# Kernel tuning notes

Hardware: AMD Instinct MI355X
Metric: run time of the kernel (lower is better)

The kernel has to match this reference:

```python
import jax, jax.numpy as jnp
import numpy as np

N_ENT, N_REL, H, DEG, TOPK = 150000, 500, 128, 32, 10


def setup_inputs() -> dict:
    key = jax.random.key(0)
    ks = jax.random.split(key, 8)
    return {
        "ent_emb": jax.random.normal(ks[0], (N_ENT, H), jnp.float32),
        "rel_emb": jax.random.normal(ks[1], (N_REL, H), jnp.float32),
        "W": jax.random.normal(ks[2], (H, H), jnp.float32) * 0.1,
        "W_r": jax.random.normal(ks[3], (H, H), jnp.float32) * 0.1,
        "a": jax.random.normal(ks[4], (3 * H, 1), jnp.float32) * 0.1,
        "neigh_w": jax.random.normal(ks[5], (H, H), jnp.float32) * 0.1,
        "src": jax.random.randint(ks[6], (N_ENT, DEG), 0, N_ENT),      # src node of each in-edge per dst
        "rel_id": jax.random.randint(ks[7], (N_ENT, DEG), 0, N_REL),   # relation id per edge
    }


def reference(ent_emb, rel_emb, W, W_r, a, neigh_w, src, rel_id):
    # node / relation projections
    h_node = ent_emb @ W                    # [N_ENT, H]
    h_rel = rel_emb @ W_r                   # [N_REL, H]
    # split attention vector: leaky_relu([h_src|h_dst|r] @ a) == leaky_relu(h_src@a1 + h_dst@a2 + r@a3)
    a1, a2, a3 = a[:H, 0], a[H:2 * H, 0], a[2 * H:, 0]
    s_src = h_node @ a1                     # [N_ENT]
    s_dst = h_node @ a2                     # [N_ENT]
    s_rel = h_rel @ a3                      # [N_REL]

    # edge scores on full graph; dst of row i is node i
    score = jax.nn.leaky_relu(s_src[src] + s_dst[:, None] + s_rel[rel_id], 0.2)  # [N_ENT, DEG]

    # top-k incoming edges per destination (dgl.sampling.select_topk, edge_dir='in')
    _, top_idx = jax.lax.top_k(score, TOPK)                 # [N_ENT, TOPK]
    src_k = jnp.take_along_axis(src, top_idx, axis=1)       # [N_ENT, TOPK]
    rel_k = jnp.take_along_axis(rel_id, top_idx, axis=1)

    # recompute attention on sampled subgraph + edge softmax per destination
    e = jax.nn.leaky_relu(s_src[src_k] + s_dst[:, None] + s_rel[rel_k], 0.2)     # [N_ENT, TOPK]
    attn = jax.nn.softmax(e, axis=1)

    # composition (add) of gathered src features with relation features, weighted scatter-sum
    comp = h_node[src_k] + h_rel[rel_k]                     # [N_ENT, TOPK, H]
    neigh = jnp.einsum('nkh,nk->nh', comp, attn)            # weighted sum over in-edges

    out = jnp.tanh(neigh @ neigh_w)                         # bn=None, dropout=eval identity
    return out
```

## Files before the change

### kernel.cpp

```cpp
#include <hip/hip_runtime.h>
#include <hip/hip_bf16.h>
#include <math.h>

#define N_ENT 150000
#define N_REL 500
#define H     128
#define DEG   32
#define TOPK  10

typedef unsigned short ushort_t;
typedef unsigned int   uint_t;
typedef __attribute__((ext_vector_type(8))) short short8;
typedef __attribute__((ext_vector_type(4))) float f32x4;

__device__ inline ushort_t f2bf(float x) {
    __hip_bfloat16 h = __float2bfloat16(x);
    return *reinterpret_cast<ushort_t*>(&h);
}
__device__ inline float bf2f(ushort_t u) {
    uint_t v = ((uint_t)u) << 16;
    return *reinterpret_cast<float*>(&v);
}
__device__ inline float dot4(float4 a, float4 b) {
    return a.x * b.x + a.y * b.y + a.z * b.z + a.w * b.w;
}
__device__ inline float fast_tanh(float x) {
    float e = __expf(2.f * x);
    return 1.f - 2.f * __builtin_amdgcn_rcpf(e + 1.f);
}

__global__ __launch_bounds__(128) void precompute_small(
    const float* __restrict__ W, const float* __restrict__ Wr,
    const float* __restrict__ nw, const float* __restrict__ a,
    float* __restrict__ M, float* __restrict__ M2,
    float* __restrict__ v1, float* __restrict__ v2, float* __restrict__ u3)
{
    int j = threadIdx.x;
    if (blockIdx.x < H) {
        int r = blockIdx.x;
        float m = 0.f, m2 = 0.f;
        for (int t = 0; t < H; ++t) {
            float x = nw[t * H + j];
            m  += W [r * H + t] * x;
            m2 += Wr[r * H + t] * x;
        }
        M [r * H + j] = m;
        M2[r * H + j] = m2;
    } else {
        int h = j;
        float s1 = 0.f, s2 = 0.f, s3 = 0.f;
        for (int t = 0; t < H; ++t) {
            s1 += W [h * H + t] * a[t];
            s2 += W [h * H + t] * a[H + t];
            s3 += Wr[h * H + t] * a[2 * H + t];
        }
        v1[h] = s1; v2[h] = s2; u3[h] = s3;
    }
}

__global__ __launch_bounds__(64) void bfrag_build(
    const float* __restrict__ M, ushort_t* __restrict__ Bhi,
    ushort_t* __restrict__ Blo)
{
    int b = blockIdx.x;
    int c = b >> 2, tt = b & 3;
    int l = threadIdx.x;
    int n  = c * 16 + (l & 15);
    int k0 = tt * 32 + (l >> 4) * 8;
    #pragma unroll
    for (int j = 0; j < 8; ++j) {
        float x = M[(k0 + j) * H + n];
        ushort_t h = f2bf(x);
        Bhi[(size_t)(b * 64 + l) * 8 + j] = h;
        Blo[(size_t)(b * 64 + l) * 8 + j] = f2bf(x - bf2f(h));
    }
}

__global__ __launch_bounds__(128) void rel_transform(
    const float* __restrict__ rel, const float* __restrict__ M2,
    const float* __restrict__ u3, ushort_t* __restrict__ Rb,
    float* __restrict__ srel)
{
    __shared__ float red[H];
    int r = blockIdx.x, j = threadIdx.x;
    float acc = 0.f;
    for (int h = 0; h < H; ++h)
        acc += rel[r * H + h] * M2[h * H + j];
    Rb[r * H + j] = f2bf(acc);
    red[j] = rel[r * H + j] * u3[j];
    __syncthreads();
    for (int s = 64; s > 0; s >>= 1) {
        if (j < s) red[j] += red[j + s];
        __syncthreads();
    }
    if (j == 0) srel[r] = red[0];
}

__global__ __launch_bounds__(256) void ent_transform3(
    const float* __restrict__ ent, const ushort_t* __restrict__ Bhi,
    const ushort_t* __restrict__ Blo, const float* __restrict__ v1,
    const float* __restrict__ v2, ushort_t* __restrict__ Gb,
    float* __restrict__ ssrc, float* __restrict__ sdst)
{
    const int t    = threadIdx.x;
    const int w    = t >> 6;
    const int l    = t & 63;
    const int m    = l & 15;
    const int quad = l >> 4;
    const long blockRow = (long)blockIdx.x * 128;
    const long waveRow  = blockRow + (long)w * 32;

    float4 v1a[4], v1b[4], v2a[4], v2b[4];
    #pragma unroll
    for (int tt = 0; tt < 4; ++tt) {
        const float* p1 = v1 + tt * 32 + quad * 8;
        const float* p2 = v2 + tt * 32 + quad * 8;
        v1a[tt] = *(const float4*)p1; v1b[tt] = *(const float4*)(p1 + 4);
        v2a[tt] = *(const float4*)p2; v2b[tt] = *(const float4*)(p2 + 4);
    }

    short8 Ahi[2][4], Alo[2][4];
    float p1s[2] = {0.f, 0.f}, p2s[2] = {0.f, 0.f};
    #pragma unroll
    for (int s = 0; s < 2; ++s) {
        long row = waveRow + s * 16 + m;
        long rc  = row < N_ENT ? row : (N_ENT - 1);
        const float* rp = ent + rc * H;
        #pragma unroll
        for (int tt = 0; tt < 4; ++tt) {
            float4 e0 = *(const float4*)(rp + tt * 32 + quad * 8);
            float4 e1 = *(const float4*)(rp + tt * 32 + quad * 8 + 4);
            p1s[s] += dot4(e0, v1a[tt]) + dot4(e1, v1b[tt]);
            p2s[s] += dot4(e0, v2a[tt]) + dot4(e1, v2b[tt]);
            float x[8] = {e0.x, e0.y, e0.z, e0.w, e1.x, e1.y, e1.z, e1.w};
            #pragma unroll
            for (int j = 0; j < 8; ++j) {
                ushort_t h = f2bf(x[j]);
                Ahi[s][tt][j] = (short)h;
                Alo[s][tt][j] = (short)f2bf(x[j] - bf2f(h));
            }
        }
    }
    #pragma unroll
    for (int s = 0; s < 2; ++s) {
        p1s[s] += __shfl_xor(p1s[s], 16); p1s[s] += __shfl_xor(p1s[s], 32);
        p2s[s] += __shfl_xor(p2s[s], 16); p2s[s] += __shfl_xor(p2s[s], 32);
    }
    if (quad == 0) {
        #pragma unroll
        for (int s = 0; s < 2; ++s) {
            long row = waveRow + s * 16 + m;
            if (row < N_ENT) { ssrc[row] = p1s[s]; sdst[row] = p2s[s]; }
        }
    }

    for (int c = 0; c < 8; ++c) {
        short8 bh[4], bl[4];
        #pragma unroll
        for (int tt = 0; tt < 4; ++tt) {
            size_t off = (size_t)((c * 4 + tt) * 64 + l) * 8;
            bh[tt] = *(const short8*)(Bhi + off);
            bl[tt] = *(const short8*)(Blo + off);
        }
        f32x4 acc0 = {0.f, 0.f, 0.f, 0.f}, acc1 = {0.f, 0.f, 0.f, 0.f};
        #pragma unroll
        for (int tt = 0; tt < 4; ++tt) {
            acc0 = __builtin_amdgcn_mfma_f32_16x16x32_bf16(Ahi[0][tt], bh[tt], acc0, 0, 0, 0);
            acc0 = __builtin_amdgcn_mfma_f32_16x16x32_bf16(Alo[0][tt], bh[tt], acc0, 0, 0, 0);
            acc0 = __builtin_amdgcn_mfma_f32_16x16x32_bf16(Ahi[0][tt], bl[tt], acc0, 0, 0, 0);
            acc1 = __builtin_amdgcn_mfma_f32_16x16x32_bf16(Ahi[1][tt], bh[tt], acc1, 0, 0, 0);
            acc1 = __builtin_amdgcn_mfma_f32_16x16x32_bf16(Alo[1][tt], bh[tt], acc1, 0, 0, 0);
            acc1 = __builtin_amdgcn_mfma_f32_16x16x32_bf16(Ahi[1][tt], bl[tt], acc1, 0, 0, 0);
        }
        #pragma unroll
        for (int s = 0; s < 2; ++s) {
            f32x4 a = s ? acc1 : acc0;
            #pragma unroll
            for (int r = 0; r < 4; ++r) {
                long row = waveRow + s * 16 + quad * 4 + r;
                if (row < N_ENT)
                    Gb[row * H + c * 16 + m] = f2bf(a[r]);
            }
        }
    }
}

__global__ __launch_bounds__(256) void gather_topk_out(
    const int* __restrict__ src, const int* __restrict__ rel_id,
    const float* __restrict__ ssrc, const float* __restrict__ sdst,
    const float* __restrict__ srel, const ushort_t* __restrict__ Gb,
    const ushort_t* __restrict__ Rb, float* __restrict__ out)
{
    int l   = threadIdx.x & 31;
    int hw  = (blockIdx.x * blockDim.x + threadIdx.x) >> 5;
    int nhw = (gridDim.x * blockDim.x) >> 5;
    for (int i = hw; i < N_ENT; i += nhw) {
        int sidx = src   [(size_t)i * DEG + l];
        int ridx = rel_id[(size_t)i * DEG + l];
        float x   = ssrc[sidx] + sdst[i] + srel[ridx];
        float val = x >= 0.f ? x : 0.2f * x;

        float curv = val;
        float tvv[TOPK]; int ts[TOPK], tr[TOPK];
        #pragma unroll
        for (int k = 0; k < TOPK; ++k) {
            float v = curv; int id = l;
            #pragma unroll
            for (int off = 1; off < 32; off <<= 1) {
                float v2 = __shfl_xor(v, off, 32);
                int   i2 = __shfl_xor(id, off, 32);
                if (v2 > v || (v2 == v && i2 < id)) { v = v2; id = i2; }
            }
            tvv[k] = v;
            ts[k] = __shfl(sidx, id, 32);
            tr[k] = __shfl(ridx, id, 32);
            if (l == id) curv = -INFINITY;
        }

        float mx = tvv[0], wsum = 0.f, wk[TOPK];
        #pragma unroll
        for (int k = 0; k < TOPK; ++k) { wk[k] = __expf(tvv[k] - mx); wsum += wk[k]; }
        float inv = __builtin_amdgcn_rcpf(wsum);

        float4 acc = {0.f, 0.f, 0.f, 0.f};
        #pragma unroll
        for (int k = 0; k < TOPK; ++k) {
            float w = wk[k] * inv;
            ushort4 gv = *(const ushort4*)(Gb + (size_t)ts[k] * H + l * 4);
            ushort4 rv = *(const ushort4*)(Rb + (size_t)tr[k] * H + l * 4);
            acc.x += w * (bf2f(gv.x) + bf2f(rv.x));
            acc.y += w * (bf2f(gv.y) + bf2f(rv.y));
            acc.z += w * (bf2f(gv.z) + bf2f(rv.z));
            acc.w += w * (bf2f(gv.w) + bf2f(rv.w));
        }
        float4 o;
        o.x = fast_tanh(acc.x); o.y = fast_tanh(acc.y);
        o.z = fast_tanh(acc.z); o.w = fast_tanh(acc.w);
        ((float4*)(out + (size_t)i * H))[l] = o;
    }
}

extern "C" void kernel_launch(void* const* d_in, const int* in_sizes, int n_in,
                              void* d_out, int out_size, void* d_ws, size_t ws_size,
                              hipStream_t stream) {
    const float* ent = (const float*)d_in[0];
    const float* rel = (const float*)d_in[1];
    const float* W   = (const float*)d_in[2];
    const float* Wr  = (const float*)d_in[3];
    const float* a   = (const float*)d_in[4];
    const float* nw  = (const float*)d_in[5];
    const int*   src = (const int*)d_in[6];
    const int*   rid = (const int*)d_in[7];
    float* out = (float*)d_out;

    float* ws = (float*)d_ws;
    float*    M    = ws;
    float*    M2   = M    + 16384;
    float*    v1   = M2   + 16384;
    float*    v2   = v1   + 128;
    float*    u3   = v2   + 128;
    float*    srel = u3   + 128;
    float*    ssrc = srel + 512;
    float*    sdst = ssrc + 150016;
    ushort_t* Bhi  = (ushort_t*)(sdst + 150016);
    ushort_t* Blo  = Bhi + 16384;
    ushort_t* Rb   = Blo + 16384;
    ushort_t* Gb   = Rb  + 64000;

    precompute_small<<<H + 1, H, 0, stream>>>(W, Wr, nw, a, M, M2, v1, v2, u3);
    bfrag_build    <<<32, 64, 0, stream>>>(M, Bhi, Blo);
    rel_transform  <<<N_REL, H, 0, stream>>>(rel, M2, u3, Rb, srel);
    ent_transform3 <<<(N_ENT + 127) / 128, 256, 0, stream>>>(ent, Bhi, Blo,
                                                             v1, v2, Gb, ssrc, sdst);
    gather_topk_out<<<2048, 256, 0, stream>>>(src, rid, ssrc, sdst, srel,
                                              Gb, Rb, out);
}
```

Measured before the change: 346.7 us.

## Replace iterative top-k shuffles with rank-count selection and ballot compaction

Top-k selection now has each lane count how many of the 32 edge scores rank ahead of it, instead of doing ten rounds of argmax shuffle reductions. Softmax max and sum become single butterfly reductions over the selected lanes. The selected lanes are then compacted with a ballot mask, and source and relation ids are packed into one word so each pick needs fewer shuffles. All ten gathers are issued before any accumulation, so more memory requests are in flight at once. The summation order of the softmax weights changes, and the packing assumes ids fit in 18 and 14 bits.

After: 329.4 us. 1.05x faster.

```diff
diff --git a/kernel.cpp b/kernel.cpp
--- a/kernel.cpp
+++ b/kernel.cpp
@@ -191,47 +191,66 @@
     const float* __restrict__ srel, const ushort_t* __restrict__ Gb,
     const ushort_t* __restrict__ Rb, float* __restrict__ out)
 {
-    int l   = threadIdx.x & 31;
+    const int l         = threadIdx.x & 31;
+    const int halfShift = threadIdx.x & 32;
     int hw  = (blockIdx.x * blockDim.x + threadIdx.x) >> 5;
     int nhw = (gridDim.x * blockDim.x) >> 5;
+
     for (int i = hw; i < N_ENT; i += nhw) {
         int sidx = src   [(size_t)i * DEG + l];
         int ridx = rel_id[(size_t)i * DEG + l];
         float x   = ssrc[sidx] + sdst[i] + srel[ridx];
         float val = x >= 0.f ? x : 0.2f * x;
 
-        float curv = val;
-        float tvv[TOPK]; int ts[TOPK], tr[TOPK];
+        int rank = 0;
+        #pragma unroll
+        for (int xm = 1; xm < 32; ++xm) {
+            float v2 = __shfl_xor(val, xm, 32);
+            bool ahead = (v2 > val) || (v2 == val && (l ^ xm) < l);
+            rank += ahead ? 1 : 0;
+        }
+        bool sel = rank < TOPK;
+
+        float mx = val;
+        #pragma unroll
+        for (int off = 1; off < 32; off <<= 1)
+            mx = fmaxf(mx, __shfl_xor(mx, off, 32));
+
+        float e  = sel ? __expf(val - mx) : 0.f;
+        float ws = e;
+        #pragma unroll
+        for (int off = 1; off < 32; off <<= 1)
+            ws += __shfl_xor(ws, off, 32);
+        float w = e * __builtin_amdgcn_rcpf(ws);
+
+        unsigned long long ball = __ballot(sel);
+        uint_t mask = (uint_t)(ball >> halfShift);
+
+        uint_t packed = (uint_t)sidx | ((uint_t)ridx << 18);
+        uint_t pk[TOPK]; float wk[TOPK];
         #pragma unroll
         for (int k = 0; k < TOPK; ++k) {
-            float v = curv; int id = l;
-            #pragma unroll
-            for (int off = 1; off < 32; off <<= 1) {
-                float v2 = __shfl_xor(v, off, 32);
-                int   i2 = __shfl_xor(id, off, 32);
-                if (v2 > v || (v2 == v && i2 < id)) { v = v2; id = i2; }
-            }
-            tvv[k] = v;
-            ts[k] = __shfl(sidx, id, 32);
-            tr[k] = __shfl(ridx, id, 32);
-            if (l == id) curv = -INFINITY;
-        }
-
-        float mx = tvv[0], wsum = 0.f, wk[TOPK];
-        #pragma unroll
-        for (int k = 0; k < TOPK; ++k) { wk[k] = __expf(tvv[k] - mx); wsum += wk[k]; }
-        float inv = __builtin_amdgcn_rcpf(wsum);
-
+            int lk = (int)__builtin_ctz(mask); mask &= mask - 1;
+            pk[k] = (uint_t)__shfl((int)packed, lk, 32);
+            wk[k] = __shfl(w, lk, 32);
+        }
+
+        ushort4 gv[TOPK], rv[TOPK];
+        #pragma unroll
+        for (int k = 0; k < TOPK; ++k) {
+            size_t s_k = pk[k] & 0x3FFFF;
+            size_t r_k = pk[k] >> 18;
+            gv[k] = *(const ushort4*)(Gb + s_k * H + l * 4);
+            rv[k] = *(const ushort4*)(Rb + r_k * H + l * 4);
+        }
         float4 acc = {0.f, 0.f, 0.f, 0.f};
         #pragma unroll
         for (int k = 0; k < TOPK; ++k) {
-            float w = wk[k] * inv;
-            ushort4 gv = *(const ushort4*)(Gb + (size_t)ts[k] * H + l * 4);
-            ushort4 rv = *(const ushort4*)(Rb + (size_t)tr[k] * H + l * 4);
-            acc.x += w * (bf2f(gv.x) + bf2f(rv.x));
-            acc.y += w * (bf2f(gv.y) + bf2f(rv.y));
-            acc.z += w * (bf2f(gv.z) + bf2f(rv.z));
-            acc.w += w * (bf2f(gv.w) + bf2f(rv.w));
+            float wv = wk[k];
+            acc.x += wv * (bf2f(gv[k].x) + bf2f(rv[k].x));
+            acc.y += wv * (bf2f(gv[k].y) + bf2f(rv[k].y));
+            acc.z += wv * (bf2f(gv[k].z) + bf2f(rv[k].z));
+            acc.w += wv * (bf2f(gv[k].w) + bf2f(rv[k].w));
         }
         float4 o;
         o.x = fast_tanh(acc.x); o.y = fast_tanh(acc.y);
```
